# Kernel tuning notes

Measured on AMD Instinct MI355X. Metric: run time of the kernel, lower is better.

Reference implementation:

```python
import jax, jax.numpy as jnp
import numpy as np

BATCH = 4096
IN_FEATURES = 8192
OUT_FEATURES = 8192
N_GROUPS = 1024  # non-overlapping value ranges partitioning [-4, 4]


def setup_inputs() -> dict:
    key = jax.random.key(0)
    k1, k2, k3 = jax.random.split(key, 3)
    x = jax.random.normal(k1, (BATCH, IN_FEATURES), dtype=jnp.float32)
    # Range index metadata (sorted by min, non-overlapping, as _build_range_index assumes)
    edges = jnp.linspace(-4.0, 4.0, N_GROUPS + 1).astype(jnp.float32)
    mins = edges[:-1]
    maxs = edges[1:]
    # Each group owns a full IN_FEATURES-wide weight row in the flat NVMe buffer
    start_pos = jnp.zeros((N_GROUPS,), dtype=jnp.int32)
    sizes = jnp.full((N_GROUPS,), IN_FEATURES, dtype=jnp.int32)
    offsets = (jnp.arange(N_GROUPS, dtype=jnp.int32) * IN_FEATURES)
    weights_flat = jax.random.normal(k2, (N_GROUPS * IN_FEATURES,), dtype=jnp.float32) * 0.02
    # Which output neurons have any metadata entry (others are skipped -> stay 0)
    out_mask = jax.random.randint(k3, (OUT_FEATURES,), 0, 2) > 0
    return {"x": x, "weights_flat": weights_flat, "mins": mins, "maxs": maxs,
            "start_pos": start_pos, "offsets": offsets, "sizes": sizes, "out_mask": out_mask}


def reference(x, weights_flat, mins, maxs, start_pos, offsets, sizes, out_mask):
    B, IN = x.shape
    OUT = out_mask.shape[0]
    G = mins.shape[0]
    # input_val per position: x[:, i].mean() (equals x[0, i] when B == 1)
    val = jnp.mean(x, axis=0)  # [IN]
    # binary search over sorted non-overlapping [min, max] ranges
    g = jnp.searchsorted(mins, val, side='right').astype(jnp.int32) - 1  # [IN]
    gc = jnp.clip(g, 0, G - 1)
    hit = (g >= 0) & (val >= mins[gc]) & (val <= maxs[gc])
    # weight lookup: pos_in_group = in_idx - start_pos, bounds-checked
    pos = jnp.arange(IN, dtype=jnp.int32) - start_pos[gc]
    pos_ok = (pos >= 0) & (pos < sizes[gc])
    idx = jnp.clip(offsets[gc] + pos, 0, weights_flat.shape[0] - 1)
    w = jnp.where(hit & pos_ok, weights_flat[idx], jnp.float32(0))
    # inner MAC loop is independent of out_idx -> same scalar for every covered neuron
    s = jnp.sum(val * w)
    row0 = jnp.where(out_mask, s, jnp.float32(0))  # [OUT]
    out = jnp.zeros((B, OUT), dtype=x.dtype).at[0].set(row0)
    return out
```

## Files before the change

### kernel.cpp

```cpp
#include <hip/hip_runtime.h>

#define BATCH 4096
#define IN_F 8192
#define OUT_F 8192
#define NG 1024
#define NW (NG * IN_F)
#define ROWS_PER_BLK 16

__global__ __launch_bounds__(256) void colsum_kernel(const float* __restrict__ x,
                                                     float* __restrict__ colsum) {
    const int col4 = (blockIdx.x * 256 + threadIdx.x);
    const int row0 = blockIdx.y * ROWS_PER_BLK;
    const float4* __restrict__ xp = (const float4*)x;
    const int stride4 = IN_F / 4;
    long long base = (long long)row0 * stride4 + col4;
    float4 v[ROWS_PER_BLK];
#pragma unroll
    for (int r = 0; r < ROWS_PER_BLK; ++r)
        v[r] = xp[base + (long long)r * stride4];
    float a0 = 0.f, a1 = 0.f, a2 = 0.f, a3 = 0.f;
#pragma unroll
    for (int r = 0; r < ROWS_PER_BLK; ++r) {
        a0 += v[r].x; a1 += v[r].y; a2 += v[r].z; a3 += v[r].w;
    }
    float* dst = colsum + col4 * 4;
    atomicAdd(dst + 0, a0);
    atomicAdd(dst + 1, a1);
    atomicAdd(dst + 2, a2);
    atomicAdd(dst + 3, a3);
}

__global__ __launch_bounds__(256) void scalar_kernel(const float* __restrict__ colsum,
                                                     const float* __restrict__ mins,
                                                     const float* __restrict__ maxs,
                                                     const int* __restrict__ start_pos,
                                                     const int* __restrict__ offsets,
                                                     const int* __restrict__ sizes,
                                                     const float* __restrict__ wflat,
                                                     const unsigned char* __restrict__ mask_raw,
                                                     float* __restrict__ ws_scalars) {
    __shared__ float smins[NG];
    __shared__ int sstart[NG];
    __shared__ int soffs[NG];
    __shared__ int ssize[NG];
    __shared__ float sred[256];
    const int t = threadIdx.x;
    for (int i = t; i < NG; i += 256) {
        smins[i]  = mins[i];
        sstart[i] = start_pos[i];
        soffs[i]  = offsets[i];
        ssize[i]  = sizes[i];
    }
    __syncthreads();

    const int j = blockIdx.x * 256 + t;
    float val = colsum[j] * (1.0f / (float)BATCH);
    int lo = 0, hi = NG;
    while (lo < hi) {
        int mid = (lo + hi) >> 1;
        if (smins[mid] <= val) lo = mid + 1; else hi = mid;
    }
    int g = lo - 1;
    float local = 0.f;
    if (g >= 0 && val >= smins[g] && val <= maxs[g]) {
        int pos = j - sstart[g];
        if (pos >= 0 && pos < ssize[g]) {
            long long idx = (long long)soffs[g] + (long long)pos;
            if (idx < 0) idx = 0;
            if (idx > (long long)(NW - 1)) idx = NW - 1;
            local = val * wflat[idx];
        }
    }
    sred[t] = local;
    __syncthreads();
    for (int ofs = 128; ofs > 0; ofs >>= 1) {
        if (t < ofs) sred[t] += sred[t + ofs];
        __syncthreads();
    }
    if (t == 0) atomicAdd(&ws_scalars[0], sred[0]);

    if (blockIdx.x == 0) {
        const int* mi = (const int*)mask_raw;
        int ok = 1;
#pragma unroll
        for (int i = 0; i < 8; ++i) {
            int v = mi[t * 8 + i];
            ok &= (v == 0 || v == 1) ? 1 : 0;
        }
        __syncthreads();
        ((unsigned long long)0);
        __shared__ int sflag[256];
        sflag[t] = ok;
        __syncthreads();
        for (int ofs = 128; ofs > 0; ofs >>= 1) {
            if (t < ofs) sflag[t] &= sflag[t + ofs];
            __syncthreads();
        }
        if (t == 0) ((int*)ws_scalars)[1] = sflag[0];
    }
}

__global__ __launch_bounds__(256) void out_kernel(const unsigned char* __restrict__ mask_raw,
                                                  const float* __restrict__ ws_scalars,
                                                  float4* __restrict__ out4) {
    const long long total4 = (long long)BATCH * OUT_F / 4;
    const long long stride = (long long)gridDim.x * blockDim.x;
    long long i = (long long)blockIdx.x * blockDim.x + threadIdx.x;
    const float s = ws_scalars[0];
    const int mask_is_i32 = ((const int*)ws_scalars)[1];
    for (; i < total4; i += stride) {
        float4 v = make_float4(0.f, 0.f, 0.f, 0.f);
        if (i < OUT_F / 4) {
            const int j = (int)i * 4;
            int m0, m1, m2, m3;
            if (mask_is_i32) {
                const int* mi = (const int*)mask_raw;
                m0 = mi[j]; m1 = mi[j + 1]; m2 = mi[j + 2]; m3 = mi[j + 3];
            } else {
                m0 = mask_raw[j]; m1 = mask_raw[j + 1];
                m2 = mask_raw[j + 2]; m3 = mask_raw[j + 3];
            }
            v.x = m0 ? s : 0.f; v.y = m1 ? s : 0.f;
            v.z = m2 ? s : 0.f; v.w = m3 ? s : 0.f;
        }
        out4[i] = v;
    }
}

extern "C" void kernel_launch(void* const* d_in, const int* in_sizes, int n_in,
                              void* d_out, int out_size, void* d_ws, size_t ws_size,
                              hipStream_t stream) {
    const float* x          = (const float*)d_in[0];
    const float* wflat      = (const float*)d_in[1];
    const float* mins       = (const float*)d_in[2];
    const float* maxs       = (const float*)d_in[3];
    const int*   start_pos  = (const int*)d_in[4];
    const int*   offsets    = (const int*)d_in[5];
    const int*   sizes      = (const int*)d_in[6];
    const unsigned char* mask = (const unsigned char*)d_in[7];

    float* colsum     = (float*)d_ws;
    float* ws_scalars = colsum + IN_F;

    hipMemsetAsync(colsum, 0, IN_F * sizeof(float) + 8, stream);

    colsum_kernel<<<dim3(IN_F / (256 * 4), BATCH / ROWS_PER_BLK), 256, 0, stream>>>(x, colsum);
    scalar_kernel<<<IN_F / 256, 256, 0, stream>>>(colsum, mins, maxs, start_pos, offsets,
                                                  sizes, wflat, mask, ws_scalars);
    out_kernel<<<2048, 256, 0, stream>>>(mask, ws_scalars, (float4*)d_out);
}
```

Baseline: 275.5 us.

## Replace atomic column and scalar reductions with deterministic partial-sum buffers

The column-sum kernel now writes per-chunk float4 partial sums to a workspace buffer instead of issuing float atomicAdds, and the scalar kernel sums 256 partials per column itself. The per-block scalar results are also stored in an array that the output kernel reduces, instead of being combined with an atomic. This drops the memset launch and the atomic contention, and makes the result deterministic. In exchange it writes and rereads an 8 MB partial buffer, and each of the 8192 scalar-kernel threads does a 256-step strided loop.

```diff
diff --git a/kernel.cpp b/kernel.cpp
--- a/kernel.cpp
+++ b/kernel.cpp
@@ -5,15 +5,17 @@
 #define OUT_F 8192
 #define NG 1024
 #define NW (NG * IN_F)
+#define RCHUNKS 256
 #define ROWS_PER_BLK 16
 
+
 __global__ __launch_bounds__(256) void colsum_kernel(const float* __restrict__ x,
-                                                     float* __restrict__ colsum) {
-    const int col4 = (blockIdx.x * 256 + threadIdx.x);
-    const int row0 = blockIdx.y * ROWS_PER_BLK;
+                                                     float4* __restrict__ part4) {
+    const int col4 = blockIdx.x * 256 + threadIdx.x;
+    const int y = blockIdx.y;
     const float4* __restrict__ xp = (const float4*)x;
     const int stride4 = IN_F / 4;
-    long long base = (long long)row0 * stride4 + col4;
+    long long base = (long long)(y * ROWS_PER_BLK) * stride4 + col4;
     float4 v[ROWS_PER_BLK];
 #pragma unroll
     for (int r = 0; r < ROWS_PER_BLK; ++r)
@@ -23,14 +25,10 @@
     for (int r = 0; r < ROWS_PER_BLK; ++r) {
         a0 += v[r].x; a1 += v[r].y; a2 += v[r].z; a3 += v[r].w;
     }
-    float* dst = colsum + col4 * 4;
-    atomicAdd(dst + 0, a0);
-    atomicAdd(dst + 1, a1);
-    atomicAdd(dst + 2, a2);
-    atomicAdd(dst + 3, a3);
+    part4[(long long)y * stride4 + col4] = make_float4(a0, a1, a2, a3);
 }
 
-__global__ __launch_bounds__(256) void scalar_kernel(const float* __restrict__ colsum,
+__global__ __launch_bounds__(256) void scalar_kernel(const float* __restrict__ part,
                                                      const float* __restrict__ mins,
                                                      const float* __restrict__ maxs,
                                                      const int* __restrict__ start_pos,
@@ -38,7 +36,8 @@
                                                      const int* __restrict__ sizes,
                                                      const float* __restrict__ wflat,
                                                      const unsigned char* __restrict__ mask_raw,
-                                                     float* __restrict__ ws_scalars) {
+                                                     float* __restrict__ spart,
+                                                     int* __restrict__ flag) {
     __shared__ float smins[NG];
     __shared__ int sstart[NG];
     __shared__ int soffs[NG];
@@ -54,7 +53,12 @@
     __syncthreads();
 
     const int j = blockIdx.x * 256 + t;
-    float val = colsum[j] * (1.0f / (float)BATCH);
+    float csum = 0.f;
+#pragma unroll 8
+    for (int y = 0; y < RCHUNKS; ++y)
+        csum += part[(long long)y * IN_F + j];
+    float val = csum * (1.0f / (float)BATCH);
+
     int lo = 0, hi = NG;
     while (lo < hi) {
         int mid = (lo + hi) >> 1;
@@ -77,7 +81,7 @@
         if (t < ofs) sred[t] += sred[t + ofs];
         __syncthreads();
     }
-    if (t == 0) atomicAdd(&ws_scalars[0], sred[0]);
+    if (t == 0) spart[blockIdx.x] = sred[0];
 
     if (blockIdx.x == 0) {
         const int* mi = (const int*)mask_raw;
@@ -87,8 +91,6 @@
             int v = mi[t * 8 + i];
             ok &= (v == 0 || v == 1) ? 1 : 0;
         }
-        __syncthreads();
-        ((unsigned long long)0);
         __shared__ int sflag[256];
         sflag[t] = ok;
         __syncthreads();
@@ -96,21 +98,28 @@
             if (t < ofs) sflag[t] &= sflag[t + ofs];
             __syncthreads();
         }
-        if (t == 0) ((int*)ws_scalars)[1] = sflag[0];
+        if (t == 0) *flag = sflag[0];
     }
 }
 
 __global__ __launch_bounds__(256) void out_kernel(const unsigned char* __restrict__ mask_raw,
-                                                  const float* __restrict__ ws_scalars,
+                                                  const float* __restrict__ spart,
+                                                  const int* __restrict__ flag,
                                                   float4* __restrict__ out4) {
     const long long total4 = (long long)BATCH * OUT_F / 4;
     const long long stride = (long long)gridDim.x * blockDim.x;
     long long i = (long long)blockIdx.x * blockDim.x + threadIdx.x;
-    const float s = ws_scalars[0];
-    const int mask_is_i32 = ((const int*)ws_scalars)[1];
     for (; i < total4; i += stride) {
         float4 v = make_float4(0.f, 0.f, 0.f, 0.f);
         if (i < OUT_F / 4) {
+            const float4* sp4 = (const float4*)spart;
+            float4 p0 = sp4[0], p1 = sp4[1], p2 = sp4[2], p3 = sp4[3];
+            float4 p4 = sp4[4], p5 = sp4[5], p6 = sp4[6], p7 = sp4[7];
+            float s = ((p0.x + p0.y + p0.z + p0.w) + (p1.x + p1.y + p1.z + p1.w))
+                    + ((p2.x + p2.y + p2.z + p2.w) + (p3.x + p3.y + p3.z + p3.w))
+                    + ((p4.x + p4.y + p4.z + p4.w) + (p5.x + p5.y + p5.z + p5.w))
+                    + ((p6.x + p6.y + p6.z + p6.w) + (p7.x + p7.y + p7.z + p7.w));
+            const int mask_is_i32 = *flag;
             const int j = (int)i * 4;
             int m0, m1, m2, m3;
             if (mask_is_i32) {
@@ -139,13 +148,12 @@
     const int*   sizes      = (const int*)d_in[6];
     const unsigned char* mask = (const unsigned char*)d_in[7];
 
-    float* colsum     = (float*)d_ws;
-    float* ws_scalars = colsum + IN_F;
+    float* part   = (float*)d_ws;
+    float* spart  = part + (long long)RCHUNKS * IN_F;
+    int*   flag   = (int*)(spart + 32);
 
-    hipMemsetAsync(colsum, 0, IN_F * sizeof(float) + 8, stream);
-
-    colsum_kernel<<<dim3(IN_F / (256 * 4), BATCH / ROWS_PER_BLK), 256, 0, stream>>>(x, colsum);
-    scalar_kernel<<<IN_F / 256, 256, 0, stream>>>(colsum, mins, maxs, start_pos, offsets,
-                                                  sizes, wflat, mask, ws_scalars);
-    out_kernel<<<2048, 256, 0, stream>>>(mask, ws_scalars, (float4*)d_out);
+    colsum_kernel<<<dim3(IN_F / (256 * 4), RCHUNKS), 256, 0, stream>>>(x, (float4*)part);
+    scalar_kernel<<<IN_F / 256, 256, 0, stream>>>(part, mins, maxs, start_pos, offsets,
+                                                  sizes, wflat, mask, spart, flag);
+    out_kernel<<<2048, 256, 0, stream>>>(mask, spart, flag, (float4*)d_out);
 }
```

Result: no change. 274.8 us (-0.3%).
